# Kernel optimization log

Measured on AMD Instinct MI355X. Metric: run time of the kernel, lower is better.

Reference implementation:

```python
import jax, jax.numpy as jnp
from jax import lax
import numpy as np

B, CIN, COUT, D, TDIM, E = 2, 16, 8, 96, 256, 8


def setup_inputs() -> dict:
    key = jax.random.key(0)
    ks = jax.random.split(key, 12)
    s = lambda fan: 1.0 / np.sqrt(fan)
    return {
        "x": jax.random.normal(ks[0], (B, CIN, D, D, D), jnp.float32),
        "text_features": jax.random.normal(ks[1], (B, TDIM), jnp.float32),
        # expert weight basis [E, Cout, Cin, 3, 3, 3] (kaiming-uniform-ish)
        "weight_basis": jax.random.uniform(ks[2], (E, COUT, CIN, 3, 3, 3), jnp.float32, -s(CIN * 27), s(CIN * 27)),
        "bias_basis": jnp.zeros((E, COUT), jnp.float32),
        # router MLP: text_dim -> 64 -> E
        "r_w1": jax.random.uniform(ks[3], (TDIM, 64), jnp.float32, -s(TDIM), s(TDIM)),
        "r_b1": jax.random.uniform(ks[4], (64,), jnp.float32, -s(TDIM), s(TDIM)),
        "r_w2": jax.random.uniform(ks[5], (64, E), jnp.float32, -s(64), s(64)),
        "r_b2": jax.random.uniform(ks[6], (E,), jnp.float32, -s(64), s(64)),
        # modulator MLP: text_dim -> 64 -> Cout
        "m_w1": jax.random.uniform(ks[7], (TDIM, 64), jnp.float32, -s(TDIM), s(TDIM)),
        "m_b1": jax.random.uniform(ks[8], (64,), jnp.float32, -s(TDIM), s(TDIM)),
        "m_w2": jax.random.uniform(ks[9], (64, COUT), jnp.float32, -s(64), s(64)),
        "m_b2": jax.random.uniform(ks[10], (COUT,), jnp.float32, -s(64), s(64)),
    }


def reference(x, text_features, weight_basis, bias_basis,
              r_w1, r_b1, r_w2, r_b2, m_w1, m_b1, m_w2, m_b2):
    b, cin = x.shape[0], x.shape[1]
    cout = weight_basis.shape[1]
    # router -> softmax routing weights over experts
    h = jax.nn.leaky_relu(text_features @ r_w1 + r_b1, 0.1)
    router_logits = h @ r_w2 + r_b2                      # [b, E]
    routing_weights = jax.nn.softmax(router_logits, -1)  # [b, E]
    # modulator -> per-sample channel gates
    g = jax.nn.leaky_relu(text_features @ m_w1 + m_b1, 0.1)
    gamma = jax.nn.sigmoid(g @ m_w2 + m_b2)              # [b, Cout]
    # per-sample dynamic conv weights via expert mixing
    cw = jnp.einsum('be,eoixyz->boixyz', routing_weights, weight_basis)  # [b,Cout,Cin,3,3,3]
    cb = routing_weights @ bias_basis                                    # [b, Cout]
    # grouped-conv trick: batch folded into channels, groups=b
    xr = x.reshape(1, b * cin, *x.shape[2:])
    wr = cw.reshape(b * cout, cin, 3, 3, 3)
    out = lax.conv_general_dilated(
        xr, wr, window_strides=(1, 1, 1), padding=[(1, 1)] * 3,
        dimension_numbers=('NCDHW', 'OIDHW', 'NCDHW'), feature_group_count=b)
    out = out.reshape(b, cout, *out.shape[2:]) + cb[:, :, None, None, None]
    out = out * (1.0 + gamma[:, :, None, None, None])
    return out, router_logits, routing_weights
```

## Files before the change

kernel.cpp:

```cpp
#include <hip/hip_runtime.h>
#include <math.h>

#define NB 2
#define CIN 16
#define COUT 8
#define DD 96
#define TDIM 256
#define NE 8
#define VOX (DD*DD*DD)
#define OUT_ELEMS (NB*COUT*VOX)

#define XT_BYTES ((size_t)NB * VOX * 32)
#define WS_A_F 7168
#define WS_D_F 7184

#define LX 18
#define PLANE (LX*LX)
#define NVX (PLANE*5)
#define HALFB (NVX*16)

#define TV 1024
#define NTB (VOX/TV)

#define MWN (COUT*CIN*27)

typedef _Float16 f16x8 __attribute__((ext_vector_type(8)));
typedef _Float16 f16x4 __attribute__((ext_vector_type(4)));
typedef float f32x4 __attribute__((ext_vector_type(4)));

__global__ __launch_bounds__(256) void transpose_setup(
    const float* __restrict__ x, _Float16* __restrict__ xt,
    const float* __restrict__ text,
    const float* __restrict__ wb,
    const float* __restrict__ bb,
    const float* __restrict__ rw1, const float* __restrict__ rb1,
    const float* __restrict__ rw2, const float* __restrict__ rb2,
    const float* __restrict__ mw1, const float* __restrict__ mb1,
    const float* __restrict__ mw2, const float* __restrict__ mb2,
    float* __restrict__ dout_tail,
    char* __restrict__ tab)
{
    __shared__ union {
        _Float16 buf[CIN][TV];
        struct {
            float mw[MWN];
            float part[256];
            float hg[2][64];
            float logits[NE];
            float rwv[NE];
        } s;
    } u;
    const int t = threadIdx.x;
    const int b = blockIdx.y;

    if (blockIdx.x == NTB) {
        {
            const int o = t & 127;
            const int which = o >> 6, j = o & 63;
            const int kh = t >> 7;
            const float* __restrict__ w1 = which ? mw1 : rw1;
            const float* __restrict__ tx = text + b*TDIM + kh*128;
            const float* __restrict__ wp = w1 + (size_t)(kh*128)*64 + j;
            float a0 = 0.f, a1 = 0.f, a2 = 0.f, a3 = 0.f;
            #pragma unroll 8
            for (int k = 0; k < 128; k += 4) {
                a0 = fmaf(tx[k+0], wp[(k+0)*64], a0);
                a1 = fmaf(tx[k+1], wp[(k+1)*64], a1);
                a2 = fmaf(tx[k+2], wp[(k+2)*64], a2);
                a3 = fmaf(tx[k+3], wp[(k+3)*64], a3);
            }
            u.s.part[t] = (a0 + a1) + (a2 + a3);
        }
        __syncthreads();
        if (t < 128) {
            const int which = t >> 6, j = t & 63;
            float acc = (which ? mb1 : rb1)[j] + u.s.part[t] + u.s.part[t + 128];
            u.s.hg[which][j] = (acc >= 0.f) ? acc : 0.1f * acc;
        }
        __syncthreads();
        if (t < NE) {
            float acc = rb2[t];
            #pragma unroll
            for (int k = 0; k < 64; ++k) acc = fmaf(u.s.hg[0][k], rw2[k*NE + t], acc);
            u.s.logits[t] = acc;
            dout_tail[b*NE + t] = acc;
        }
        __syncthreads();
        if (t < NE) {
            float mx = u.s.logits[0];
            for (int k = 1; k < NE; ++k) mx = fmaxf(mx, u.s.logits[k]);
            float ssum = 0.f;
            for (int k = 0; k < NE; ++k) ssum += expf(u.s.logits[k] - mx);
            const float w = expf(u.s.logits[t] - mx) / ssum;
            u.s.rwv[t] = w;
            dout_tail[NB*NE + b*NE + t] = w;
        }
        __syncthreads();
        float rv[NE];
        #pragma unroll
        for (int e = 0; e < NE; ++e) rv[e] = u.s.rwv[e];

        if (t < COUT) {
            float acc = mb2[t];
            #pragma unroll
            for (int k = 0; k < 64; ++k) acc = fmaf(u.s.hg[1][k], mw2[k*COUT + t], acc);
            const float gamma = 1.f / (1.f + expf(-acc));
            const float a = 1.f + gamma;
            float cb = 0.f;
            #pragma unroll
            for (int e = 0; e < NE; ++e) cb = fmaf(rv[e], bb[e*COUT + t], cb);
            ((float*)tab)[WS_A_F + b*COUT + t] = a;
            ((float*)tab)[WS_D_F + b*COUT + t] = cb * a;
        }

        #pragma unroll
        for (int i0 = 0; i0 < (MWN + 255)/256; ++i0) {
            const int i = i0*256 + t;
            if (i < MWN) {
                float v = 0.f;
                #pragma unroll
                for (int e = 0; e < NE; ++e) v = fmaf(rv[e], wb[e*MWN + i], v);
                u.s.mw[i] = v;
            }
        }
        __syncthreads();

        for (int r = t; r < 14*64*8; r += 256) {
            const int c  = r >> 9;
            const int l  = (r >> 3) & 63;
            const int j  = r & 7;
            const int q  = l >> 4;
            const int n  = l & 15;
            const int p  = q & 1;
            const int ci = (q >> 1)*8 + j;
            int tap;
            if (c < 9)        tap = (c/3)*9 + (c%3)*3 + p;
            else if (c < 12)  tap = (c-9)*9 + p*3 + 2;
            else if (c == 12) tap = p*9 + 8;
            else              tap = p ? -1 : 26;
            float v = 0.f;
            if (n < 8 && tap >= 0) v = u.s.mw[(n*CIN + ci)*27 + tap];
            ((_Float16*)tab)[b*7168 + r] = (_Float16)v;
        }
        return;
    }

    const int v0 = blockIdx.x * TV;
    const float* __restrict__ xb = x + (size_t)b * CIN * VOX + v0;

    #pragma unroll
    for (int ci = 0; ci < CIN; ++ci) {
        const float4 f = ((const float4*)(xb + (size_t)ci * VOX))[t];
        f16x4 hv;
        hv[0] = (_Float16)f.x; hv[1] = (_Float16)f.y;
        hv[2] = (_Float16)f.z; hv[3] = (_Float16)f.w;
        *(f16x4*)&u.buf[ci][t*4] = hv;
    }
    __syncthreads();

    #pragma unroll
    for (int i = 0; i < TV/256; ++i) {
        const int v = i*256 + t;
        union { _Float16 h[16]; uint4 uu[2]; } o;
        #pragma unroll
        for (int ci = 0; ci < CIN; ++ci) o.h[ci] = u.buf[ci][v];
        uint4* __restrict__ dst = (uint4*)(xt + (size_t)(b*VOX + v0 + v) * 16);
        dst[0] = o.uu[0];
        dst[1] = o.uu[1];
    }
}

__global__ __launch_bounds__(256) void conv_mfma(
    const _Float16* __restrict__ xt,
    const char* __restrict__ tab,
    float* __restrict__ out)
{
    __shared__ char lds[2*HALFB];
    const int tid  = threadIdx.x;
    const int lane = tid & 63;
    const int wv   = tid >> 6;
    const int b    = blockIdx.z;
    const int z0   = blockIdx.y * 3;
    const int xti  = blockIdx.x % 6;
    const int yti  = blockIdx.x / 6;
    const int x0   = xti * 16, y0 = yti * 16;

    const f16x8* __restrict__ bfp = (const f16x8*)tab;
    f16x8 bfrag[14];
    #pragma unroll
    for (int c = 0; c < 14; ++c)
        bfrag[c] = bfp[(b*14 + c)*64 + lane];

    const _Float16* __restrict__ xtb = xt + (size_t)b * VOX * 16;
    for (int s = tid; s < NVX; s += 256) {
        const int lz = s / PLANE;
        const int r1 = s - lz * PLANE;
        const int ly = r1 / LX;
        const int lx = r1 - ly * LX;
        const int zg = z0 - 1 + lz, yg = y0 - 1 + ly, xg = x0 - 1 + lx;
        const bool ok = ((unsigned)zg < 96u) & ((unsigned)yg < 96u) & ((unsigned)xg < 96u);
        const int zc = ok ? zg : 0, yc = ok ? yg : 0, xc = ok ? xg : 0;
        const uint4* __restrict__ p = (const uint4*)(xtb + (size_t)((zc*DD + yc)*DD + xc) * 16);
        uint4 lo = {0,0,0,0}, hi = {0,0,0,0};
        if (ok) { lo = p[0]; hi = p[1]; }
        *(uint4*)&lds[s*16]         = lo;
        *(uint4*)&lds[HALFB + s*16] = hi;
    }
    __syncthreads();

    const int q    = lane >> 4;
    const int m    = lane & 15;
    const int pbit = q & 1;
    const int hbit = q >> 1;

    const float* tabf = (const float*)tab;
    const float a_n = tabf[WS_A_F + b*8 + (m & 7)];
    const float d_n = tabf[WS_D_F + b*8 + (m & 7)];

    const int com = hbit*HALFB + m*16;
    const int dA = pbit*16;
    const int dB = pbit*288;
    const int dC = pbit*5184;

    #define LD_A(p_, dy_)  (*(const f16x8*)&lds[((p_)*PLANE + (yi+(dy_))*LX)*16 + com + dA])
    #define LD_G(p_)       (*(const f16x8*)&lds[((p_)*PLANE + yi*LX + 2)*16 + com + dB])
    #define LD_H12(zi_)    (*(const f16x8*)&lds[((zi_)*PLANE + (yi+2)*LX + 2)*16 + com + dC])
    #define LD_H13(zi_)    (*(const f16x8*)&lds[(((zi_)+2)*PLANE + (yi+2)*LX + 2)*16 + com])

    #pragma unroll
    for (int yi4 = 0; yi4 < 4; ++yi4) {
        const int yi = wv*4 + yi4;

        f16x8 A[3][3], G[3];
        #pragma unroll
        for (int dy = 0; dy < 3; ++dy) { A[0][dy] = LD_A(0, dy); A[1][dy] = LD_A(1, dy); }
        G[0] = LD_G(0); G[1] = LD_G(1);

        #pragma unroll
        for (int zi = 0; zi < 3; ++zi) {
            #pragma unroll
            for (int dy = 0; dy < 3; ++dy) A[2][dy] = LD_A(zi+2, dy);
            G[2] = LD_G(zi+2);
            const f16x8 H12v = LD_H12(zi);
            const f16x8 H13v = LD_H13(zi);

            f32x4 acc0 = {0.f,0.f,0.f,0.f}, acc1 = {0.f,0.f,0.f,0.f};
            acc0 = __builtin_amdgcn_mfma_f32_16x16x32_f16(A[0][0], bfrag[0],  acc0, 0,0,0);
            acc1 = __builtin_amdgcn_mfma_f32_16x16x32_f16(A[0][1], bfrag[1],  acc1, 0,0,0);
            acc0 = __builtin_amdgcn_mfma_f32_16x16x32_f16(A[0][2], bfrag[2],  acc0, 0,0,0);
            acc1 = __builtin_amdgcn_mfma_f32_16x16x32_f16(A[1][0], bfrag[3],  acc1, 0,0,0);
            acc0 = __builtin_amdgcn_mfma_f32_16x16x32_f16(A[1][1], bfrag[4],  acc0, 0,0,0);
            acc1 = __builtin_amdgcn_mfma_f32_16x16x32_f16(A[1][2], bfrag[5],  acc1, 0,0,0);
            acc0 = __builtin_amdgcn_mfma_f32_16x16x32_f16(A[2][0], bfrag[6],  acc0, 0,0,0);
            acc1 = __builtin_amdgcn_mfma_f32_16x16x32_f16(A[2][1], bfrag[7],  acc1, 0,0,0);
            acc0 = __builtin_amdgcn_mfma_f32_16x16x32_f16(A[2][2], bfrag[8],  acc0, 0,0,0);
            acc1 = __builtin_amdgcn_mfma_f32_16x16x32_f16(G[0],    bfrag[9],  acc1, 0,0,0);
            acc0 = __builtin_amdgcn_mfma_f32_16x16x32_f16(G[1],    bfrag[10], acc0, 0,0,0);
            acc1 = __builtin_amdgcn_mfma_f32_16x16x32_f16(G[2],    bfrag[11], acc1, 0,0,0);
            acc0 = __builtin_amdgcn_mfma_f32_16x16x32_f16(H12v,    bfrag[12], acc0, 0,0,0);
            acc1 = __builtin_amdgcn_mfma_f32_16x16x32_f16(H13v,    bfrag[13], acc1, 0,0,0);

            if (m < 8) {
                const int zz = z0 + zi, yy = y0 + yi;
                float* __restrict__ op = out + (size_t)(b*COUT + m)*VOX
                                            + (size_t)(zz*DD + yy)*DD + x0 + q*4;
                f32x4 res;
                #pragma unroll
                for (int r = 0; r < 4; ++r) res[r] = fmaf(acc0[r] + acc1[r], a_n, d_n);
                *reinterpret_cast<f32x4*>(op) = res;
            }

            #pragma unroll
            for (int dy = 0; dy < 3; ++dy) { A[0][dy] = A[1][dy]; A[1][dy] = A[2][dy]; }
            G[0] = G[1]; G[1] = G[2];
        }
    }
    #undef LD_A
    #undef LD_G
    #undef LD_H12
    #undef LD_H13
}

extern "C" void kernel_launch(void* const* d_in, const int* in_sizes, int n_in,
                              void* d_out, int out_size, void* d_ws, size_t ws_size,
                              hipStream_t stream) {
    const float* x    = (const float*)d_in[0];
    const float* text = (const float*)d_in[1];
    const float* wb   = (const float*)d_in[2];
    const float* bb   = (const float*)d_in[3];
    const float* rw1  = (const float*)d_in[4];
    const float* rb1  = (const float*)d_in[5];
    const float* rw2  = (const float*)d_in[6];
    const float* rb2  = (const float*)d_in[7];
    const float* mw1  = (const float*)d_in[8];
    const float* mb1  = (const float*)d_in[9];
    const float* mw2  = (const float*)d_in[10];
    const float* mb2  = (const float*)d_in[11];

    float* out = (float*)d_out;
    _Float16* xt = (_Float16*)d_ws;
    char* tab = (char*)d_ws + XT_BYTES;

    transpose_setup<<<dim3(NTB + 1, NB), 256, 0, stream>>>(
        x, xt, text, wb, bb, rw1, rb1, rw2, rb2, mw1, mb1, mw2, mb2,
        out + OUT_ELEMS, tab);

    conv_mfma<<<dim3(36, 32, NB), 256, 0, stream>>>(xt, tab, out);
}
```

Before: 251.4 us.

## Fuse NCDHW-to-channel-last fp16 transpose into conv halo load

Removes the separate transpose pass that wrote an fp16 channel-last copy of x to workspace. The conv kernel now gathers the 16 channels per voxel straight from the fp32 NCDHW input while filling LDS, converting to fp16 on the fly. This avoids one full write and re-read of the input. The cost is scalar, channel-strided loads in the halo fill and about 1.4x halo re-reading of fp32 data, four times larger than the previous 32-byte vector loads.

```diff
diff --git a/kernel.cpp b/kernel.cpp
--- a/kernel.cpp
+++ b/kernel.cpp
@@ -10,7 +10,6 @@
 #define VOX (DD*DD*DD)
 #define OUT_ELEMS (NB*COUT*VOX)
 
-#define XT_BYTES ((size_t)NB * VOX * 32)
 #define WS_A_F 7168
 #define WS_D_F 7184
 
@@ -19,17 +18,13 @@
 #define NVX (PLANE*5)
 #define HALFB (NVX*16)
 
-#define TV 1024
-#define NTB (VOX/TV)
-
 #define MWN (COUT*CIN*27)
 
 typedef _Float16 f16x8 __attribute__((ext_vector_type(8)));
 typedef _Float16 f16x4 __attribute__((ext_vector_type(4)));
 typedef float f32x4 __attribute__((ext_vector_type(4)));
 
-__global__ __launch_bounds__(256) void transpose_setup(
-    const float* __restrict__ x, _Float16* __restrict__ xt,
+__global__ __launch_bounds__(256) void setup_kernel(
     const float* __restrict__ text,
     const float* __restrict__ wb,
     const float* __restrict__ bb,
@@ -40,138 +35,108 @@
     float* __restrict__ dout_tail,
     char* __restrict__ tab)
 {
-    __shared__ union {
-        _Float16 buf[CIN][TV];
-        struct {
-            float mw[MWN];
-            float part[256];
-            float hg[2][64];
-            float logits[NE];
-            float rwv[NE];
-        } s;
-    } u;
+    __shared__ struct {
+        float mw[MWN];
+        float part[256];
+        float hg[2][64];
+        float logits[NE];
+        float rwv[NE];
+    } s;
     const int t = threadIdx.x;
-    const int b = blockIdx.y;
-
-    if (blockIdx.x == NTB) {
-        {
-            const int o = t & 127;
-            const int which = o >> 6, j = o & 63;
-            const int kh = t >> 7;
-            const float* __restrict__ w1 = which ? mw1 : rw1;
-            const float* __restrict__ tx = text + b*TDIM + kh*128;
-            const float* __restrict__ wp = w1 + (size_t)(kh*128)*64 + j;
-            float a0 = 0.f, a1 = 0.f, a2 = 0.f, a3 = 0.f;
-            #pragma unroll 8
-            for (int k = 0; k < 128; k += 4) {
-                a0 = fmaf(tx[k+0], wp[(k+0)*64], a0);
-                a1 = fmaf(tx[k+1], wp[(k+1)*64], a1);
-                a2 = fmaf(tx[k+2], wp[(k+2)*64], a2);
-                a3 = fmaf(tx[k+3], wp[(k+3)*64], a3);
-            }
-            u.s.part[t] = (a0 + a1) + (a2 + a3);
-        }
-        __syncthreads();
-        if (t < 128) {
-            const int which = t >> 6, j = t & 63;
-            float acc = (which ? mb1 : rb1)[j] + u.s.part[t] + u.s.part[t + 128];
-            u.s.hg[which][j] = (acc >= 0.f) ? acc : 0.1f * acc;
-        }
-        __syncthreads();
-        if (t < NE) {
-            float acc = rb2[t];
-            #pragma unroll
-            for (int k = 0; k < 64; ++k) acc = fmaf(u.s.hg[0][k], rw2[k*NE + t], acc);
-            u.s.logits[t] = acc;
-            dout_tail[b*NE + t] = acc;
-        }
-        __syncthreads();
-        if (t < NE) {
-            float mx = u.s.logits[0];
-            for (int k = 1; k < NE; ++k) mx = fmaxf(mx, u.s.logits[k]);
-            float ssum = 0.f;
-            for (int k = 0; k < NE; ++k) ssum += expf(u.s.logits[k] - mx);
-            const float w = expf(u.s.logits[t] - mx) / ssum;
-            u.s.rwv[t] = w;
-            dout_tail[NB*NE + b*NE + t] = w;
-        }
-        __syncthreads();
-        float rv[NE];
-        #pragma unroll
-        for (int e = 0; e < NE; ++e) rv[e] = u.s.rwv[e];
-
-        if (t < COUT) {
-            float acc = mb2[t];
-            #pragma unroll
-            for (int k = 0; k < 64; ++k) acc = fmaf(u.s.hg[1][k], mw2[k*COUT + t], acc);
-            const float gamma = 1.f / (1.f + expf(-acc));
-            const float a = 1.f + gamma;
-            float cb = 0.f;
-            #pragma unroll
-            for (int e = 0; e < NE; ++e) cb = fmaf(rv[e], bb[e*COUT + t], cb);
-            ((float*)tab)[WS_A_F + b*COUT + t] = a;
-            ((float*)tab)[WS_D_F + b*COUT + t] = cb * a;
-        }
-
-        #pragma unroll
-        for (int i0 = 0; i0 < (MWN + 255)/256; ++i0) {
-            const int i = i0*256 + t;
-            if (i < MWN) {
-                float v = 0.f;
-                #pragma unroll
-                for (int e = 0; e < NE; ++e) v = fmaf(rv[e], wb[e*MWN + i], v);
-                u.s.mw[i] = v;
-            }
-        }
-        __syncthreads();
-
-        for (int r = t; r < 14*64*8; r += 256) {
-            const int c  = r >> 9;
-            const int l  = (r >> 3) & 63;
-            const int j  = r & 7;
-            const int q  = l >> 4;
-            const int n  = l & 15;
-            const int p  = q & 1;
-            const int ci = (q >> 1)*8 + j;
-            int tap;
-            if (c < 9)        tap = (c/3)*9 + (c%3)*3 + p;
-            else if (c < 12)  tap = (c-9)*9 + p*3 + 2;
-            else if (c == 12) tap = p*9 + 8;
-            else              tap = p ? -1 : 26;
+    const int b = blockIdx.x;
+
+    {
+        const int o = t & 127;
+        const int which = o >> 6, j = o & 63;
+        const int kh = t >> 7;
+        const float* __restrict__ w1 = which ? mw1 : rw1;
+        const float* __restrict__ tx = text + b*TDIM + kh*128;
+        const float* __restrict__ wp = w1 + (size_t)(kh*128)*64 + j;
+        float a0 = 0.f, a1 = 0.f, a2 = 0.f, a3 = 0.f;
+        #pragma unroll 8
+        for (int k = 0; k < 128; k += 4) {
+            a0 = fmaf(tx[k+0], wp[(k+0)*64], a0);
+            a1 = fmaf(tx[k+1], wp[(k+1)*64], a1);
+            a2 = fmaf(tx[k+2], wp[(k+2)*64], a2);
+            a3 = fmaf(tx[k+3], wp[(k+3)*64], a3);
+        }
+        s.part[t] = (a0 + a1) + (a2 + a3);
+    }
+    __syncthreads();
+    if (t < 128) {
+        const int which = t >> 6, j = t & 63;
+        float acc = (which ? mb1 : rb1)[j] + s.part[t] + s.part[t + 128];
+        s.hg[which][j] = (acc >= 0.f) ? acc : 0.1f * acc;
+    }
+    __syncthreads();
+    if (t < NE) {
+        float acc = rb2[t];
+        #pragma unroll
+        for (int k = 0; k < 64; ++k) acc = fmaf(s.hg[0][k], rw2[k*NE + t], acc);
+        s.logits[t] = acc;
+        dout_tail[b*NE + t] = acc;
+    }
+    __syncthreads();
+    if (t < NE) {
+        float mx = s.logits[0];
+        for (int k = 1; k < NE; ++k) mx = fmaxf(mx, s.logits[k]);
+        float ssum = 0.f;
+        for (int k = 0; k < NE; ++k) ssum += expf(s.logits[k] - mx);
+        const float w = expf(s.logits[t] - mx) / ssum;
+        s.rwv[t] = w;
+        dout_tail[NB*NE + b*NE + t] = w;
+    }
+    __syncthreads();
+    float rv[NE];
+    #pragma unroll
+    for (int e = 0; e < NE; ++e) rv[e] = s.rwv[e];
+
+    if (t < COUT) {
+        float acc = mb2[t];
+        #pragma unroll
+        for (int k = 0; k < 64; ++k) acc = fmaf(s.hg[1][k], mw2[k*COUT + t], acc);
+        const float gamma = 1.f / (1.f + expf(-acc));
+        const float a = 1.f + gamma;
+        float cb = 0.f;
+        #pragma unroll
+        for (int e = 0; e < NE; ++e) cb = fmaf(rv[e], bb[e*COUT + t], cb);
+        ((float*)tab)[WS_A_F + b*COUT + t] = a;
+        ((float*)tab)[WS_D_F + b*COUT + t] = cb * a;
+    }
+
+    #pragma unroll
+    for (int i0 = 0; i0 < (MWN + 255)/256; ++i0) {
+        const int i = i0*256 + t;
+        if (i < MWN) {
             float v = 0.f;
-            if (n < 8 && tap >= 0) v = u.s.mw[(n*CIN + ci)*27 + tap];
-            ((_Float16*)tab)[b*7168 + r] = (_Float16)v;
-        }
-        return;
-    }
-
-    const int v0 = blockIdx.x * TV;
-    const float* __restrict__ xb = x + (size_t)b * CIN * VOX + v0;
-
-    #pragma unroll
-    for (int ci = 0; ci < CIN; ++ci) {
-        const float4 f = ((const float4*)(xb + (size_t)ci * VOX))[t];
-        f16x4 hv;
-        hv[0] = (_Float16)f.x; hv[1] = (_Float16)f.y;
-        hv[2] = (_Float16)f.z; hv[3] = (_Float16)f.w;
-        *(f16x4*)&u.buf[ci][t*4] = hv;
-    }
-    __syncthreads();
-
-    #pragma unroll
-    for (int i = 0; i < TV/256; ++i) {
-        const int v = i*256 + t;
-        union { _Float16 h[16]; uint4 uu[2]; } o;
-        #pragma unroll
-        for (int ci = 0; ci < CIN; ++ci) o.h[ci] = u.buf[ci][v];
-        uint4* __restrict__ dst = (uint4*)(xt + (size_t)(b*VOX + v0 + v) * 16);
-        dst[0] = o.uu[0];
-        dst[1] = o.uu[1];
+            #pragma unroll
+            for (int e = 0; e < NE; ++e) v = fmaf(rv[e], wb[e*MWN + i], v);
+            s.mw[i] = v;
+        }
+    }
+    __syncthreads();
+
+    for (int r = t; r < 14*64*8; r += 256) {
+        const int c  = r >> 9;
+        const int l  = (r >> 3) & 63;
+        const int j  = r & 7;
+        const int q  = l >> 4;
+        const int n  = l & 15;
+        const int p  = q & 1;
+        const int ci = (q >> 1)*8 + j;
+        int tap;
+        if (c < 9)        tap = (c/3)*9 + (c%3)*3 + p;
+        else if (c < 12)  tap = (c-9)*9 + p*3 + 2;
+        else if (c == 12) tap = p*9 + 8;
+        else              tap = p ? -1 : 26;
+        float v = 0.f;
+        if (n < 8 && tap >= 0) v = s.mw[(n*CIN + ci)*27 + tap];
+        ((_Float16*)tab)[b*7168 + r] = (_Float16)v;
     }
 }
 
 __global__ __launch_bounds__(256) void conv_mfma(
-    const _Float16* __restrict__ xt,
+    const float* __restrict__ x,
     const char* __restrict__ tab,
     float* __restrict__ out)
 {
@@ -191,20 +156,25 @@
     for (int c = 0; c < 14; ++c)
         bfrag[c] = bfp[(b*14 + c)*64 + lane];
 
-    const _Float16* __restrict__ xtb = xt + (size_t)b * VOX * 16;
-    for (int s = tid; s < NVX; s += 256) {
-        const int lz = s / PLANE;
-        const int r1 = s - lz * PLANE;
+    const float* __restrict__ xb = x + (size_t)b * CIN * VOX;
+    for (int sv = tid; sv < NVX; sv += 256) {
+        const int lz = sv / PLANE;
+        const int r1 = sv - lz * PLANE;
         const int ly = r1 / LX;
         const int lx = r1 - ly * LX;
         const int zg = z0 - 1 + lz, yg = y0 - 1 + ly, xg = x0 - 1 + lx;
         const bool ok = ((unsigned)zg < 96u) & ((unsigned)yg < 96u) & ((unsigned)xg < 96u);
-        const int zc = ok ? zg : 0, yc = ok ? yg : 0, xc = ok ? xg : 0;
-        const uint4* __restrict__ p = (const uint4*)(xtb + (size_t)((zc*DD + yc)*DD + xc) * 16);
-        uint4 lo = {0,0,0,0}, hi = {0,0,0,0};
-        if (ok) { lo = p[0]; hi = p[1]; }
-        *(uint4*)&lds[s*16]         = lo;
-        *(uint4*)&lds[HALFB + s*16] = hi;
+        union { _Float16 h[16]; uint4 uu[2]; } o;
+        o.uu[0] = make_uint4(0u,0u,0u,0u);
+        o.uu[1] = make_uint4(0u,0u,0u,0u);
+        if (ok) {
+            const float* __restrict__ gp = xb + (size_t)((zg*DD + yg)*DD + xg);
+            #pragma unroll
+            for (int ci = 0; ci < CIN; ++ci)
+                o.h[ci] = (_Float16)gp[(size_t)ci * VOX];
+        }
+        *(uint4*)&lds[sv*16]         = o.uu[0];
+        *(uint4*)&lds[HALFB + sv*16] = o.uu[1];
     }
     __syncthreads();
 
@@ -298,12 +268,11 @@
     const float* mb2  = (const float*)d_in[11];
 
     float* out = (float*)d_out;
-    _Float16* xt = (_Float16*)d_ws;
-    char* tab = (char*)d_ws + XT_BYTES;
-
-    transpose_setup<<<dim3(NTB + 1, NB), 256, 0, stream>>>(
-        x, xt, text, wb, bb, rw1, rb1, rw2, rb2, mw1, mb1, mw2, mb2,
+    char* tab = (char*)d_ws;
+
+    setup_kernel<<<dim3(NB), 256, 0, stream>>>(
+        text, wb, bb, rw1, rb1, rw2, rb2, mw1, mb1, mw2, mb2,
         out + OUT_ELEMS, tab);
 
-    conv_mfma<<<dim3(36, 32, NB), 256, 0, stream>>>(xt, tab, out);
+    conv_mfma<<<dim3(36, 32, NB), 256, 0, stream>>>(x, tab, out);
 }
```

Measured after the change: 269.6 us. +7.2%, slower.
